# Performance work log

Measured on AMD Instinct MI355X. Metric: run time of the kernel, lower is better.

Reference implementation:

```python
import jax, jax.numpy as jnp
import numpy as np

DILATIONS = (3, 6, 12, 18, 24)
B, C, H, W = 16, 26, 96, 72
INNER = 128
EPS = 1e-5


def conv2d(x, w, padding=0, dilation=1):
    return jax.lax.conv_general_dilated(
        x, w, window_strides=(1, 1),
        padding=[(padding, padding), (padding, padding)],
        rhs_dilation=(dilation, dilation),
        dimension_numbers=('NCHW', 'OIHW', 'NCHW'))


def batch_norm(x, p):
    # p: [4, C] rows = (scale, bias, running_mean, running_var); eval-mode BN
    s, b, m, v = p[0], p[1], p[2], p[3]
    inv = s * jax.lax.rsqrt(v + EPS)
    return x * inv[None, :, None, None] + (b - m * inv)[None, :, None, None]


def basic_block(x, w1, p1, w2, p2, wd=None, pd=None):
    h = jax.nn.relu(batch_norm(conv2d(x, w1, padding=1), p1))
    h = batch_norm(conv2d(h, w2, padding=1), p2)
    idn = x if wd is None else batch_norm(conv2d(x, wd), pd)
    return jax.nn.relu(h + idn)


def _bilinear(img, py, px):
    # img: [cpg, H, W]; py, px: [K, H, W] sample coords; zero outside bounds
    Hi, Wi = img.shape[1], img.shape[2]
    y0f = jnp.floor(py); x0f = jnp.floor(px)
    ly = py - y0f; lx = px - x0f
    y0 = y0f.astype(jnp.int32); x0 = x0f.astype(jnp.int32)

    def gather(yi, xi):
        valid = ((yi >= 0) & (yi < Hi) & (xi >= 0) & (xi < Wi)).astype(img.dtype)
        return img[:, jnp.clip(yi, 0, Hi - 1), jnp.clip(xi, 0, Wi - 1)] * valid[None]

    return (gather(y0, x0) * ((1 - ly) * (1 - lx))[None]
            + gather(y0, x0 + 1) * ((1 - ly) * lx)[None]
            + gather(y0 + 1, x0) * (ly * (1 - lx))[None]
            + gather(y0 + 1, x0 + 1) * (ly * lx)[None])


def deform_conv(x, offset, w, dil):
    # x: [B,C,H,W]; offset: [B, dg*2*K, H, W] ((dy,dx) interleaved per kernel tap);
    # w: [O,C,3,3]; stride 1, padding = dil -> same spatial size
    Bn, Cn, Hn, Wn = x.shape
    K = w.shape[2] * w.shape[3]
    dg = offset.shape[1] // (2 * K)
    cpg = Cn // dg
    off = offset.reshape(Bn, dg, K, 2, Hn, Wn)
    ky = jnp.arange(K) // 3 - 1
    kx = jnp.arange(K) % 3 - 1
    base_y = (jnp.arange(Hn)[None, :] + ky[:, None] * dil).astype(x.dtype)  # [K,H]
    base_x = (jnp.arange(Wn)[None, :] + kx[:, None] * dil).astype(x.dtype)  # [K,W]
    py = base_y[None, None, :, :, None] + off[:, :, :, 0]  # [B,dg,K,H,W]
    px = base_x[None, None, :, None, :] + off[:, :, :, 1]
    xg = x.reshape(Bn, dg, cpg, Hn, Wn)
    samp = jax.vmap(jax.vmap(_bilinear))(xg, py, px)  # [B,dg,cpg,K,H,W]
    vals = samp.reshape(Bn, Cn, K, Hn, Wn)
    return jnp.einsum('bckij,ock->boij', vals, w.reshape(w.shape[0], Cn, K))


def setup_inputs():
    key = jax.random.key(0)
    ks = jax.random.split(key, 14)
    std = 0.001  # matches nn.init.normal_(std=0.001)

    def bnp(k, c):
        k1, k2, k3, k4 = jax.random.split(k, 4)
        return jnp.stack([jax.random.uniform(k1, (c,), minval=0.5, maxval=1.5),
                          jax.random.normal(k2, (c,)) * 0.1,
                          jax.random.normal(k3, (c,)) * 0.1,
                          jax.random.uniform(k4, (c,), minval=0.5, maxval=1.5)])

    return {
        'ref_x': jax.random.normal(ks[0], (B, C, H, W), jnp.float32),
        'sup_x': jax.random.normal(ks[1], (B, C, H, W), jnp.float32),
        'w1_0': jax.random.normal(ks[2], (INNER, C, 3, 3), jnp.float32) * std,
        'w2_0': jax.random.normal(ks[3], (INNER, INNER, 3, 3), jnp.float32) * std,
        'wd_0': jax.random.normal(ks[4], (INNER, C, 1, 1), jnp.float32) * std,
        'bn1_0': bnp(ks[5], INNER),
        'bn2_0': bnp(ks[6], INNER),
        'bnd_0': bnp(ks[7], INNER),
        'w1_rest': jax.random.normal(ks[8], (19, INNER, INNER, 3, 3), jnp.float32) * std,
        'w2_rest': jax.random.normal(ks[9], (19, INNER, INNER, 3, 3), jnp.float32) * std,
        'bn1_rest': jnp.stack([bnp(k, INNER) for k in jax.random.split(ks[10], 19)]),
        'bn2_rest': jnp.stack([bnp(k, INNER) for k in jax.random.split(ks[11], 19)]),
        'offset_ws': jax.random.normal(ks[12], (5, C * 2 * 9, INNER, 3, 3), jnp.float32) * std,
        'deform_ws': jax.random.normal(ks[13], (5, C, C, 3, 3), jnp.float32) * std,
    }


def reference(ref_x, sup_x, w1_0, w2_0, wd_0, bn1_0, bn2_0, bnd_0,
              w1_rest, w2_rest, bn1_rest, bn2_rest, offset_ws, deform_ws):
    # offset feature chain: 20 BasicBlocks on (ref - sup)
    h = basic_block(ref_x - sup_x, w1_0, bn1_0, w2_0, bn2_0, wd_0, bnd_0)
    for t in range(19):
        h = basic_block(h, w1_rest[t], bn1_rest[t], w2_rest[t], bn2_rest[t])
    # 5 dilation branches: dilated offset conv -> deformable conv on sup_x; average
    out = jnp.zeros_like(sup_x)
    for i, dil in enumerate(DILATIONS):
        off = conv2d(h, offset_ws[i], padding=dil, dilation=dil)
        out = out + deform_conv(sup_x, off, deform_ws[i], dil)
    return out / len(DILATIONS)
```

## Files before the change

kernel.cpp:

```cpp
#include <hip/hip_runtime.h>

typedef unsigned short u16;
typedef unsigned int u32;
typedef __bf16 bf16x8 __attribute__((ext_vector_type(8)));
typedef float f32x4 __attribute__((ext_vector_type(4)));

#define NB 16
#define CIN 26
#define IMH 96
#define IMW 72
#define HW6912 6912
#define NPIX 110592
#define SPH 98
#define SPW 74
#define SPAD 1

__device__ __forceinline__ float b2f(u16 h) {
    union { u32 u; float f; } x; x.u = ((u32)h) << 16; return x.f;
}
__device__ __forceinline__ u16 f2b(float f) {
    union { float f; u32 u; } x; x.f = f;
    u32 u = x.u;
    u32 r = (u + 0x7fffu + ((u >> 16) & 1u)) >> 16;
    return (u16)r;
}
__device__ __forceinline__ float ldin(const void* p, int i, int f) {
    return f ? ((const float*)p)[i] : b2f(((const u16*)p)[i]);
}

__device__ __forceinline__ int pbase(int m, int clog2) {
    int b = m / HW6912;
    int p = m - b * HW6912;
    int y = p / IMW;
    int x = p - y * IMW;
    return (((b * SPH + y + SPAD) * SPW) + (x + SPAD)) << clog2;
}

__device__ __forceinline__ void glds16(const u16* g, u16* l) {
    __builtin_amdgcn_global_load_lds(
        (const __attribute__((address_space(1))) void*)g,
        (__attribute__((address_space(3))) void*)l, 16, 0, 0);
}

__global__ void probe_kernel(const void* bn, int* flag) {
    if (threadIdx.x == 0 && blockIdx.x == 0) {
        const float* f = (const float*)bn;
        int cnt = 0;
        for (int j = 64; j < 128; ++j) {
            float v = f[j];
            if (v >= 0.4f && v <= 1.6f) cnt++;
        }
        *flag = (cnt >= 32) ? 1 : 0;
    }
}

__global__ __launch_bounds__(256) void zero_ws_kernel(uint4* p, int n16) {
    int i = blockIdx.x * 256 + threadIdx.x;
    int stride = gridDim.x * 256;
    for (; i < n16; i += stride) p[i] = make_uint4(0u, 0u, 0u, 0u);
}

__global__ __launch_bounds__(256) void fill_x0_kernel(const void* __restrict__ ref,
                                                      const void* __restrict__ sup,
                                                      u16* __restrict__ x0,
                                                      const int* __restrict__ flag) {
    int f = *flag;
    int t = blockIdx.x * 256 + threadIdx.x;
    int b = t / HW6912;
    int p = t - b * HW6912;
    int y = p / IMW;
    int x = p - y * IMW;
    int dst = ((b * SPH + y + SPAD) * SPW + (x + SPAD)) << 5;
    #pragma unroll 1
    for (int c = 0; c < CIN; ++c) {
        int src = (b * CIN + c) * HW6912 + p;
        x0[dst + c] = f2b(ldin(ref, src, f) - ldin(sup, src, f));
    }
}

__global__ __launch_bounds__(256) void prep_rest_kernel(const void* __restrict__ w1r,
                                                        const void* __restrict__ w2r,
                                                        const void* __restrict__ bn1r,
                                                        const void* __restrict__ bn2r,
                                                        u16* __restrict__ dst,
                                                        const int* __restrict__ flag) {
    int f = *flag;
    int idx = blockIdx.x * 256 + threadIdx.x;
    int c = idx / 147456;
    int e = idx - c * 147456;
    int ee = e & 7;
    int l = (e >> 3) & 63;
    int j = (e >> 9) & 1;
    int w2 = (e >> 10) & 1;
    int rest = e >> 11;
    int it = rest % 36;
    int nt = rest / 36;
    int n = nt * 64 + w2 * 32 + j * 16 + (l & 15);
    int k = it * 32 + ((l >> 4) << 3) + ee;
    int s = k >> 7, ci = k & 127;
    const void* w  = (c < 19) ? w1r : w2r;
    int wb         = ((c < 19) ? c : (c - 19)) * 147456;
    const void* bn = (c < 19) ? bn1r : bn2r;
    int bb         = ((c < 19) ? c : (c - 19)) * 512;
    float inv = ldin(bn, bb + n, f) * rsqrtf(ldin(bn, bb + 384 + n, f) + 1e-5f);
    dst[idx] = f2b(ldin(w, wb + (n * 128 + ci) * 9 + s, f) * inv);
}

__global__ __launch_bounds__(256) void prep_b0_kernel(const void* __restrict__ w1_0,
                                                      const void* __restrict__ w2_0,
                                                      const void* __restrict__ wd_0,
                                                      const void* __restrict__ bn1_0,
                                                      const void* __restrict__ bn2_0,
                                                      const void* __restrict__ bnd_0,
                                                      u16* __restrict__ W20,
                                                      u16* __restrict__ W10,
                                                      u16* __restrict__ Wd,
                                                      const int* __restrict__ flag) {
    int f = *flag;
    int idx = blockIdx.x * 256 + threadIdx.x;
    if (idx < 147456) {
        int e = idx;
        int ee = e & 7;
        int l = (e >> 3) & 63;
        int j = (e >> 9) & 1;
        int w2 = (e >> 10) & 1;
        int rest = e >> 11;
        int it = rest % 36;
        int nt = rest / 36;
        int n = nt * 64 + w2 * 32 + j * 16 + (l & 15);
        int k = it * 32 + ((l >> 4) << 3) + ee;
        int s = k >> 7, ci = k & 127;
        float inv = ldin(bn2_0, n, f) * rsqrtf(ldin(bn2_0, 384 + n, f) + 1e-5f);
        W20[idx] = f2b(ldin(w2_0, (n * 128 + ci) * 9 + s, f) * inv);
    } else if (idx < 184320) {
        int j = idx - 147456;
        int o = j / 288, k = j - o * 288;
        int s = k >> 5, ci = k & 31;
        float inv = ldin(bn1_0, o, f) * rsqrtf(ldin(bn1_0, 384 + o, f) + 1e-5f);
        W10[j] = (ci < CIN) ? f2b(ldin(w1_0, (o * CIN + ci) * 9 + s, f) * inv) : (u16)0;
    } else {
        int j = idx - 184320;
        int o = j >> 5, ci = j & 31;
        float inv = ldin(bnd_0, o, f) * rsqrtf(ldin(bnd_0, 384 + o, f) + 1e-5f);
        Wd[j] = (ci < CIN) ? f2b(ldin(wd_0, o * CIN + ci, f) * inv) : (u16)0;
    }
}

__global__ __launch_bounds__(256) void prep_off_kernel(const void* __restrict__ offw,
                                                       u16* __restrict__ dst,
                                                       const int* __restrict__ flag) {
    int f = *flag;
    int idx = blockIdx.x * 256 + threadIdx.x;
    int e = idx & 7;
    int l = (idx >> 3) & 63;
    int j = (idx >> 9) & 1;
    int w2 = (idx >> 10) & 1;
    int rest = idx >> 11;
    int it = rest % 36;
    int dnt = rest / 36;
    int nt = dnt & 7;
    int d = dnt >> 3;
    int n = nt * 64 + w2 * 32 + j * 16 + (l & 15);
    int k = it * 32 + (l >> 4) * 8 + e;
    int s = k >> 7, ci = k & 127;
    dst[idx] = (n < 468) ? f2b(ldin(offw, ((d * 468 + n) * 128 + ci) * 9 + s, f)) : (u16)0;
}

__global__ __launch_bounds__(256) void prep_dw_kernel(const void* __restrict__ dwall,
                                                      float* __restrict__ dst,
                                                      const int* __restrict__ flag) {
    int f = *flag;
    int idx = blockIdx.x * 256 + threadIdx.x;
    if (idx >= 32760) return;
    int d = idx / 6552;
    int r = idx - d * 6552;
    int o = r % 28;
    int ct = r / 28;
    int c = ct / 9, t = ct - c * 9;
    dst[idx] = (o < CIN) ? ldin(dwall, d * 6084 + (o * CIN + c) * 9 + t, f) : 0.f;
}

__global__ __launch_bounds__(256) void prep_bias_kernel(const void* __restrict__ bn1_0,
                                                        const void* __restrict__ bn2_0,
                                                        const void* __restrict__ bnd_0,
                                                        const void* __restrict__ bn1r,
                                                        const void* __restrict__ bn2r,
                                                        float* __restrict__ dst,
                                                        const int* __restrict__ flag) {
    int f = *flag;
    int idx = blockIdx.x * 256 + threadIdx.x;
    if (idx >= 41 * 128) return;
    int set = idx >> 7;
    int o = idx & 127;
    const void* bn; int bb = 0;
    if (set == 0) bn = bn1_0;
    else if (set == 1) bn = bn2_0;
    else if (set == 2) bn = bnd_0;
    else if (set < 22) { bn = bn1r; bb = (set - 3) * 512; }
    else { bn = bn2r; bb = (set - 22) * 512; }
    float s = ldin(bn, bb + o, f), b = ldin(bn, bb + 128 + o, f);
    float mu = ldin(bn, bb + 256 + o, f), v = ldin(bn, bb + 384 + o, f);
    float inv = s * rsqrtf(v + 1e-5f);
    dst[idx] = b - mu * inv;
}

__global__ __launch_bounds__(256) void conv_gemm(const u16* __restrict__ A,
                                                 const u16* __restrict__ W,
                                                 const float* __restrict__ bias,
                                                 u16* __restrict__ out,
                                                 int clog2, int nslab, int K,
                                                 int relu) {
    __shared__ u16 As[2][128 * 32];
    __shared__ u16 Bs[2][64 * 32];
    int tid = threadIdx.x;
    int m0 = blockIdx.x * 128;
    int n0 = blockIdx.y * 64;
    int Cin = 1 << clog2;

    int r0 = tid >> 2;
    int q8 = (tid & 3) * 8;
    int arow0 = pbase(m0 + r0, clog2) + q8;
    int arow1 = pbase(m0 + r0 + 64, clog2) + q8;
    int brow0 = (n0 + r0) * K + q8;
    int l8 = tid * 8;

    f32x4 acc[4][2];
    #pragma unroll
    for (int i = 0; i < 4; ++i)
        #pragma unroll
        for (int j = 0; j < 2; ++j)
            acc[i][j] = (f32x4){0.f, 0.f, 0.f, 0.f};

    int wid = tid >> 6;
    int wm = (wid >> 1) * 64;
    int wn = (wid & 1) * 32;
    int lane = tid & 63;
    int lr = lane & 15;
    int lq = lane >> 4;

    int nk = K >> 5;
    auto stage = [&](int buf, int kt) {
        int sl = kt >> clog2;
        int win = kt & (Cin - 1);
        int soff = 0;
        if (nslab == 9) {
            int d3 = sl / 3;
            soff = (((d3 - 1) * SPW + (sl - d3 * 3 - 1))) << clog2;
        }
        glds16(A + arow0 + soff + win, &As[buf][l8]);
        glds16(A + arow1 + soff + win, &As[buf][2048 + l8]);
        glds16(W + brow0 + kt, &Bs[buf][l8]);
    };

    stage(0, 0);
    #pragma unroll 1
    for (int it = 0; it < nk; ++it) {
        __syncthreads();
        if (it + 1 < nk) stage((it + 1) & 1, (it + 1) << 5);
        const u16* as = As[it & 1];
        const u16* bs = Bs[it & 1];
        bf16x8 af[4], bfr[2];
        #pragma unroll
        for (int i = 0; i < 4; ++i)
            af[i] = *(const bf16x8*)&as[(wm + i * 16 + lr) * 32 + lq * 8];
        #pragma unroll
        for (int j = 0; j < 2; ++j)
            bfr[j] = *(const bf16x8*)&bs[(wn + j * 16 + lr) * 32 + lq * 8];
        #pragma unroll
        for (int i = 0; i < 4; ++i)
            #pragma unroll
            for (int j = 0; j < 2; ++j)
                acc[i][j] = __builtin_amdgcn_mfma_f32_16x16x32_bf16(af[i], bfr[j], acc[i][j], 0, 0, 0);
    }

    #pragma unroll
    for (int i = 0; i < 4; ++i) {
        #pragma unroll
        for (int r = 0; r < 4; ++r) {
            int ml = m0 + wm + i * 16 + lq * 4 + r;
            int ob = pbase(ml, 7);
            #pragma unroll
            for (int j = 0; j < 2; ++j) {
                int n = n0 + wn + j * 16 + lr;
                float v = acc[i][j][r] + bias[n];
                if (relu) v = fmaxf(v, 0.f);
                out[ob + n] = f2b(v);
            }
        }
    }
}

__global__ __launch_bounds__(256, 8) void chain_conv(const u16* __restrict__ A,
                                                     const u16* __restrict__ W,
                                                     const float* __restrict__ bias,
                                                     const u16* __restrict__ idn,
                                                     u16* __restrict__ out,
                                                     int relu) {
    __shared__ u16 As[2][128 * 32];
    int tid = threadIdx.x;
    int wg = blockIdx.x;
    int sw = (wg & 7) * 216 + (wg >> 3);
    int mt = sw >> 1, nt = sw & 1;
    int m0 = mt * 128, n0 = nt * 64;

    int r0 = tid >> 2;
    int q8 = (tid & 3) * 8;
    int pbq[2];
    #pragma unroll
    for (int q = 0; q < 2; ++q) {
        int p = m0 + r0 + q * 64;
        int b = p / HW6912;
        int rem = p - b * HW6912;
        int y = rem / IMW;
        int x = rem - y * IMW;
        pbq[q] = ((b * SPH + y + 1) * SPW + (x + 1)) * 128;
    }
    int l8 = tid * 8;

    f32x4 acc[4][2];
    #pragma unroll
    for (int i = 0; i < 4; ++i) {
        acc[i][0] = (f32x4){0.f, 0.f, 0.f, 0.f};
        acc[i][1] = (f32x4){0.f, 0.f, 0.f, 0.f};
    }

    int wid = tid >> 6;
    int wm = (wid >> 1) * 64;
    int w2 = wid & 1;
    int wn = w2 * 32;
    int lane = tid & 63;
    int lr = lane & 15;
    int lq = lane >> 4;

    const u16* wv = W + nt * 73728 + w2 * 1024 + lane * 8;

    auto stage = [&](int buf, int kt) {
        int sl = kt >> 7;
        int win = kt & 127;
        int d3 = sl / 3;
        int soff = ((d3 - 1) * SPW + (sl - d3 * 3 - 1)) * 128;
        glds16(A + pbq[0] + soff + win + q8, &As[buf][l8]);
        glds16(A + pbq[1] + soff + win + q8, &As[buf][2048 + l8]);
    };

    stage(0, 0);
    #pragma unroll 1
    for (int it = 0; it < 36; ++it) {
        __syncthreads();
        if (it + 1 < 36) stage((it + 1) & 1, (it + 1) << 5);
        const u16* as = As[it & 1];
        bf16x8 af[4], bfr[2];
        #pragma unroll
        for (int i = 0; i < 4; ++i)
            af[i] = *(const bf16x8*)&as[(wm + i * 16 + lr) * 32 + lq * 8];
        bfr[0] = *(const bf16x8*)(wv + it * 2048);
        bfr[1] = *(const bf16x8*)(wv + it * 2048 + 512);
        #pragma unroll
        for (int i = 0; i < 4; ++i)
            #pragma unroll
            for (int j = 0; j < 2; ++j)
                acc[i][j] = __builtin_amdgcn_mfma_f32_16x16x32_bf16(af[i], bfr[j], acc[i][j], 0, 0, 0);
    }

    #pragma unroll
    for (int i = 0; i < 4; ++i) {
        #pragma unroll
        for (int r = 0; r < 4; ++r) {
            int ml = m0 + wm + i * 16 + lq * 4 + r;
            int ob = pbase(ml, 7);
            #pragma unroll
            for (int j = 0; j < 2; ++j) {
                int n = n0 + wn + j * 16 + lr;
                float v = acc[i][j][r] + bias[n];
                if (idn) v += b2f(idn[ob + n]);
                if (relu) v = fmaxf(v, 0.f);
                out[ob + n] = f2b(v);
            }
        }
    }
}

__global__ __launch_bounds__(256, 8) void off_conv(const u16* __restrict__ A,
                                                   const u16* __restrict__ W,
                                                   u16* __restrict__ out,
                                                   int dil, int m_base) {
    __shared__ u16 As[2][128 * 32];
    int tid = threadIdx.x;
    int wg = blockIdx.x;
    int sw = (wg & 7) * 216 + (wg >> 3);
    int mt = sw >> 3, nt = sw & 7;
    int m0 = mt * 128, n0 = nt * 64;

    int r0 = tid >> 2;
    int q8 = (tid & 3) * 8;
    int pb2[2], py[2], px[2];
    #pragma unroll
    for (int q = 0; q < 2; ++q) {
        int p = m_base + m0 + r0 + q * 64;
        int b = p / HW6912;
        int rem = p - b * HW6912;
        pb2[q] = b;
        py[q] = rem / IMW;
        px[q] = rem - py[q] * IMW;
    }
    int l8 = tid * 8;

    f32x4 acc[4][2];
    #pragma unroll
    for (int i = 0; i < 4; ++i) {
        acc[i][0] = (f32x4){0.f, 0.f, 0.f, 0.f};
        acc[i][1] = (f32x4){0.f, 0.f, 0.f, 0.f};
    }

    int wid = tid >> 6;
    int wm = (wid >> 1) * 64;
    int wn = (wid & 1) * 32;
    int lane = tid & 63;
    int lr = lane & 15;
    int lq = lane >> 4;

    const u16* wv = W + nt * 73728 + (wid & 1) * 1024 + lane * 8;

    auto stage = [&](int buf, int kt) {
        int sl = kt >> 7;
        int win = kt & 127;
        int d3 = sl / 3;
        int dy = (d3 - 1) * dil, dx = (sl - d3 * 3 - 1) * dil;
        #pragma unroll
        for (int q = 0; q < 2; ++q) {
            int y2 = py[q] + dy, x2 = px[q] + dx;
            uint4 v = make_uint4(0u, 0u, 0u, 0u);
            if (y2 >= 0 && y2 < IMH && x2 >= 0 && x2 < IMW)
                v = *(const uint4*)(A + ((pb2[q] * SPH + y2 + 1) * SPW + x2 + 1) * 128 + win + q8);
            *(uint4*)&As[buf][q * 2048 + l8] = v;
        }
    };

    stage(0, 0);
    #pragma unroll 1
    for (int it = 0; it < 36; ++it) {
        __syncthreads();
        if (it + 1 < 36) stage((it + 1) & 1, (it + 1) << 5);
        const u16* as = As[it & 1];
        bf16x8 af[4], bfr[2];
        #pragma unroll
        for (int i = 0; i < 4; ++i)
            af[i] = *(const bf16x8*)&as[(wm + i * 16 + lr) * 32 + lq * 8];
        bfr[0] = *(const bf16x8*)(wv + it * 2048);
        bfr[1] = *(const bf16x8*)(wv + it * 2048 + 512);
        #pragma unroll
        for (int i = 0; i < 4; ++i)
            #pragma unroll
            for (int j = 0; j < 2; ++j)
                acc[i][j] = __builtin_amdgcn_mfma_f32_16x16x32_bf16(af[i], bfr[j], acc[i][j], 0, 0, 0);
    }

    #pragma unroll
    for (int i = 0; i < 4; ++i) {
        #pragma unroll
        for (int r = 0; r < 4; ++r) {
            int ml = m0 + wm + i * 16 + lq * 4 + r;
            int ob = ml * 468;
            #pragma unroll
            for (int j = 0; j < 2; ++j) {
                int n = n0 + wn + j * 16 + lr;
                if (n < 468) out[ob + n] = f2b(acc[i][j][r]);
            }
        }
    }
}

template <int F>
__device__ __forceinline__ float dsamp2(const void* sup, int base, int yi, int xi) {
    bool ok = (yi >= 0) & (yi < IMH) & (xi >= 0) & (xi < IMW);
    int yc = yi < 0 ? 0 : (yi > IMH - 1 ? IMH - 1 : yi);
    int xc = xi < 0 ? 0 : (xi > IMW - 1 ? IMW - 1 : xi);
    float v = F ? ((const float*)sup)[base + yc * IMW + xc]
                : b2f(((const u16*)sup)[base + yc * IMW + xc]);
    return ok ? v : 0.f;
}

template <int F>
__device__ __forceinline__ void deform_body(const void* __restrict__ sup,
                                            const u16* __restrict__ oc,
                                            const float* __restrict__ wsm,
                                            f32x4 acc[7],
                                            int c0, int c1, int b, int y, int x, int dil) {
    #pragma unroll 1
    for (int c = c0; c < c1; ++c) {
        int ibase = (b * CIN + c) * HW6912;
        #pragma unroll
        for (int t = 0; t < 9; ++t) {
            u32 pr = *(const u32*)(oc + c * 18 + t * 2);
            float dy = b2f((u16)(pr & 0xffffu));
            float dx = b2f((u16)(pr >> 16));
            float py = (float)(y + (t / 3 - 1) * dil) + dy;
            float px = (float)(x + (t % 3 - 1) * dil) + dx;
            float y0f = floorf(py), x0f = floorf(px);
            float ly = py - y0f, lx = px - x0f;
            int y0 = (int)y0f, x0 = (int)x0f;
            float v00 = dsamp2<F>(sup, ibase, y0, x0);
            float v01 = dsamp2<F>(sup, ibase, y0, x0 + 1);
            float v10 = dsamp2<F>(sup, ibase, y0 + 1, x0);
            float v11 = dsamp2<F>(sup, ibase, y0 + 1, x0 + 1);
            float val = (v00 * (1.f - lx) + v01 * lx) * (1.f - ly)
                      + (v10 * (1.f - lx) + v11 * lx) * ly;
            const float4* wr = (const float4*)&wsm[(c * 9 + t) * 28];
            #pragma unroll
            for (int u = 0; u < 7; ++u) {
                float4 w4 = wr[u];
                acc[u][0] = fmaf(val, w4.x, acc[u][0]);
                acc[u][1] = fmaf(val, w4.y, acc[u][1]);
                acc[u][2] = fmaf(val, w4.z, acc[u][2]);
                acc[u][3] = fmaf(val, w4.w, acc[u][3]);
            }
        }
    }
}

__global__ __launch_bounds__(256) void deform_kernel(const void* __restrict__ sup,
                                                     const u16* __restrict__ offb,
                                                     const float* __restrict__ wsp,
                                                     float* __restrict__ accws,
                                                     int dil, int first, int m_base,
                                                     const int* __restrict__ flag) {
    int f = *flag;
    __shared__ alignas(16) float wsm[26 * 9 * 28];
    __shared__ float red[4 * 32 * 27];
    int tid = threadIdx.x;
    int bid = blockIdx.x;
    int sw = (bid & 7) * 108 + (bid >> 3);
    for (int i = tid; i < 1638; i += 256)
        ((float4*)wsm)[i] = ((const float4*)wsp)[i];
    __syncthreads();

    int px = tid & 31;
    int cg = tid >> 5;
    int c0 = (cg * 26) >> 3;
    int c1 = ((cg + 1) * 26) >> 3;
    int ml = sw * 32 + px;
    int m = m_base + ml;
    int b = m / HW6912;
    int p = m - b * HW6912;
    int y = p / IMW;
    int x = p - y * IMW;

    f32x4 acc[7];
    #pragma unroll
    for (int u = 0; u < 7; ++u) acc[u] = (f32x4){0.f, 0.f, 0.f, 0.f};

    const u16* oc = offb + (size_t)ml * 468;
    if (f) deform_body<1>(sup, oc, wsm, acc, c0, c1, b, y, x, dil);
    else   deform_body<0>(sup, oc, wsm, acc, c0, c1, b, y, x, dil);

    #pragma unroll
    for (int u = 0; u < 7; ++u)
        #pragma unroll
        for (int k2 = 0; k2 < 4; ++k2) {
            float v = acc[u][k2];
            acc[u][k2] = v + __shfl_xor(v, 32);
        }

    int w = tid >> 6;
    if (!(tid & 32)) {
        float* mr = red + (w * 32 + px) * 27;
        #pragma unroll
        for (int u = 0; u < 7; ++u)
            #pragma unroll
            for (int k2 = 0; k2 < 4; ++k2) {
                int o = u * 4 + k2;
                if (o < 26) mr[o] = acc[u][k2];
            }
    }
    __syncthreads();

    int base_m = m_base + sw * 32;
    for (int v = tid; v < 32 * 26; v += 256) {
        int ppx = v / 26;
        int o = v - ppx * 26;
        float s = red[(0 * 32 + ppx) * 27 + o] + red[(1 * 32 + ppx) * 27 + o]
                + red[(2 * 32 + ppx) * 27 + o] + red[(3 * 32 + ppx) * 27 + o];
        size_t ai = (size_t)(base_m + ppx) * 32 + o;
        if (first) accws[ai] = s;
        else       accws[ai] += s;
    }
}

__global__ __launch_bounds__(256) void finalize_kernel(const float* __restrict__ accws,
                                                       void* __restrict__ out,
                                                       const int* __restrict__ flag) {
    int f = *flag;
    int q = blockIdx.x * 256 + threadIdx.x;
    int b = q / (CIN * HW6912);
    int r = q - b * (CIN * HW6912);
    int o = r / HW6912;
    int p = r - o * HW6912;
    float v = accws[(size_t)(b * HW6912 + p) * 32 + o] * 0.2f;
    if (f) ((float*)out)[q] = v;
    else   ((u16*)out)[q] = f2b(v);
}

extern "C" void kernel_launch(void* const* d_in, const int* in_sizes, int n_in,
                              void* d_out, int out_size, void* d_ws, size_t ws_size,
                              hipStream_t stream) {
    (void)in_sizes; (void)n_in; (void)out_size;
    const void* ref_x    = d_in[0];
    const void* sup_x    = d_in[1];
    const void* w1_0     = d_in[2];
    const void* w2_0     = d_in[3];
    const void* wd_0     = d_in[4];
    const void* bn1_0    = d_in[5];
    const void* bn2_0    = d_in[6];
    const void* bnd_0    = d_in[7];
    const void* w1_rest  = d_in[8];
    const void* w2_rest  = d_in[9];
    const void* bn1_rest = d_in[10];
    const void* bn2_rest = d_in[11];
    const void* offset_w = d_in[12];
    const void* deform_w = d_in[13];

    size_t o_x0    = 0;
    size_t o_h0    = o_x0 + 7426048;
    size_t o_h1s   = o_h0 + 29704192;
    size_t o_acc   = o_h1s + 29704192;
    size_t o_wrest = o_acc + 14155776;
    size_t o_w20   = o_wrest + 11206656;
    size_t o_w10   = o_w20 + 294912;
    size_t o_wd    = o_w10 + 73728;
    size_t o_woff  = o_wd + 8192;
    size_t o_bias  = o_woff + 5898240;
    size_t o_wsall = o_bias + 20992;
    size_t o_flag  = o_wsall + 131072;
    size_t o_end   = o_flag + 64;
    if (ws_size < o_end) return;

    char* ws = (char*)d_ws;
    u16* x0    = (u16*)(ws + o_x0);
    u16* h0    = (u16*)(ws + o_h0);
    u16* offb  = (u16*)(ws + o_h0);
    u16* h1s   = (u16*)(ws + o_h1s);
    float* accb = (float*)(ws + o_acc);
    u16* Wr    = (u16*)(ws + o_wrest);
    u16* W20   = (u16*)(ws + o_w20);
    u16* W10   = (u16*)(ws + o_w10);
    u16* Wd    = (u16*)(ws + o_wd);
    u16* Woff  = (u16*)(ws + o_woff);
    float* biasb = (float*)(ws + o_bias);
    float* wsall = (float*)(ws + o_wsall);
    int* flagp = (int*)(ws + o_flag);

    dim3 blk(256);

    probe_kernel<<<1, 64, 0, stream>>>(bn1_0, flagp);
    zero_ws_kernel<<<2048, blk, 0, stream>>>((uint4*)ws, (int)((7426048 + 2 * 29704192) / 16));
    fill_x0_kernel<<<432, blk, 0, stream>>>(ref_x, sup_x, x0, flagp);
    prep_rest_kernel<<<21888, blk, 0, stream>>>(w1_rest, w2_rest, bn1_rest, bn2_rest, Wr, flagp);
    prep_b0_kernel<<<736, blk, 0, stream>>>(w1_0, w2_0, wd_0, bn1_0, bn2_0, bnd_0, W20, W10, Wd, flagp);
    prep_off_kernel<<<11520, blk, 0, stream>>>(offset_w, Woff, flagp);
    prep_dw_kernel<<<128, blk, 0, stream>>>(deform_w, wsall, flagp);
    prep_bias_kernel<<<21, blk, 0, stream>>>(bn1_0, bn2_0, bnd_0, bn1_rest, bn2_rest, biasb, flagp);

    conv_gemm<<<dim3(864, 2), blk, 0, stream>>>(x0, Wd, biasb + 2 * 128, h1s, 5, 1, 32, 0);
    conv_gemm<<<dim3(864, 2), blk, 0, stream>>>(x0, W10, biasb + 0 * 128, h0, 5, 9, 288, 1);
    chain_conv<<<1728, blk, 0, stream>>>(h0, W20, biasb + 1 * 128, h1s, h1s, 1);

    for (int t = 0; t < 19; ++t) {
        const u16* wa = Wr + (size_t)t * 147456;
        const u16* wb = Wr + (size_t)(19 + t) * 147456;
        chain_conv<<<1728, blk, 0, stream>>>(h1s, wa, biasb + (3 + t) * 128, nullptr, h0, 1);
        chain_conv<<<1728, blk, 0, stream>>>(h0, wb, biasb + (22 + t) * 128, h1s, h1s, 1);
    }

    const int dils[5] = {3, 6, 12, 18, 24};
    for (int i = 0; i < 5; ++i) {
        for (int cb = 0; cb < 4; ++cb) {
            int mb = cb * 27648;
            off_conv<<<1728, blk, 0, stream>>>(h1s, Woff + (size_t)i * 589824, offb, dils[i], mb);
            deform_kernel<<<864, blk, 0, stream>>>(sup_x, offb, wsall + (size_t)i * 6552,
                                                   accb, dils[i], (i == 0) ? 1 : 0, mb, flagp);
        }
    }
    finalize_kernel<<<11232, blk, 0, stream>>>(accb, d_out, flagp);
}
```

Baseline: 3.952 ms.

## Widen chain_conv tile to full 128 output channels and swizzle LDS A tile

```diff
diff --git a/kernel.cpp b/kernel.cpp
--- a/kernel.cpp
+++ b/kernel.cpp
@@ -290,7 +290,7 @@
     }
 }
 
-__global__ __launch_bounds__(256, 8) void chain_conv(const u16* __restrict__ A,
+__global__ __launch_bounds__(256, 4) void chain_conv(const u16* __restrict__ A,
                                                      const u16* __restrict__ W,
                                                      const float* __restrict__ bias,
                                                      const u16* __restrict__ idn,
@@ -299,12 +299,11 @@
     __shared__ u16 As[2][128 * 32];
     int tid = threadIdx.x;
     int wg = blockIdx.x;
-    int sw = (wg & 7) * 216 + (wg >> 3);
-    int mt = sw >> 1, nt = sw & 1;
-    int m0 = mt * 128, n0 = nt * 64;
+    int mt = (wg & 7) * 108 + (wg >> 3);
+    int m0 = mt * 128;
 
     int r0 = tid >> 2;
-    int q8 = (tid & 3) * 8;
+    int c8 = ((tid & 3) ^ (r0 & 3)) * 8;
     int pbq[2];
     #pragma unroll
     for (int q = 0; q < 2; ++q) {
@@ -317,30 +316,30 @@
     }
     int l8 = tid * 8;
 
-    f32x4 acc[4][2];
-    #pragma unroll
-    for (int i = 0; i < 4; ++i) {
-        acc[i][0] = (f32x4){0.f, 0.f, 0.f, 0.f};
-        acc[i][1] = (f32x4){0.f, 0.f, 0.f, 0.f};
-    }
+    f32x4 acc[4][4];
+    #pragma unroll
+    for (int i = 0; i < 4; ++i)
+        #pragma unroll
+        for (int jj = 0; jj < 4; ++jj)
+            acc[i][jj] = (f32x4){0.f, 0.f, 0.f, 0.f};
 
     int wid = tid >> 6;
     int wm = (wid >> 1) * 64;
-    int w2 = wid & 1;
-    int wn = w2 * 32;
+    int wn2 = wid & 1;
     int lane = tid & 63;
     int lr = lane & 15;
     int lq = lane >> 4;
-
-    const u16* wv = W + nt * 73728 + w2 * 1024 + lane * 8;
+    int rchunk = (lq ^ (lr & 3)) * 8;
+
+    const u16* wv = W + wn2 * 73728 + lane * 8;
 
     auto stage = [&](int buf, int kt) {
         int sl = kt >> 7;
         int win = kt & 127;
         int d3 = sl / 3;
         int soff = ((d3 - 1) * SPW + (sl - d3 * 3 - 1)) * 128;
-        glds16(A + pbq[0] + soff + win + q8, &As[buf][l8]);
-        glds16(A + pbq[1] + soff + win + q8, &As[buf][2048 + l8]);
+        glds16(A + pbq[0] + soff + win + c8, &As[buf][l8]);
+        glds16(A + pbq[1] + soff + win + c8, &As[buf][2048 + l8]);
     };
 
     stage(0, 0);
@@ -349,17 +348,18 @@
         __syncthreads();
         if (it + 1 < 36) stage((it + 1) & 1, (it + 1) << 5);
         const u16* as = As[it & 1];
-        bf16x8 af[4], bfr[2];
+        bf16x8 af[4], bfr[4];
         #pragma unroll
         for (int i = 0; i < 4; ++i)
-            af[i] = *(const bf16x8*)&as[(wm + i * 16 + lr) * 32 + lq * 8];
-        bfr[0] = *(const bf16x8*)(wv + it * 2048);
-        bfr[1] = *(const bf16x8*)(wv + it * 2048 + 512);
+            af[i] = *(const bf16x8*)&as[(wm + i * 16 + lr) * 32 + rchunk];
+        #pragma unroll
+        for (int jj = 0; jj < 4; ++jj)
+            bfr[jj] = *(const bf16x8*)(wv + it * 2048 + jj * 512);
         #pragma unroll
         for (int i = 0; i < 4; ++i)
             #pragma unroll
-            for (int j = 0; j < 2; ++j)
-                acc[i][j] = __builtin_amdgcn_mfma_f32_16x16x32_bf16(af[i], bfr[j], acc[i][j], 0, 0, 0);
+            for (int jj = 0; jj < 4; ++jj)
+                acc[i][jj] = __builtin_amdgcn_mfma_f32_16x16x32_bf16(af[i], bfr[jj], acc[i][jj], 0, 0, 0);
     }
 
     #pragma unroll
@@ -369,9 +369,9 @@
             int ml = m0 + wm + i * 16 + lq * 4 + r;
             int ob = pbase(ml, 7);
             #pragma unroll
-            for (int j = 0; j < 2; ++j) {
-                int n = n0 + wn + j * 16 + lr;
-                float v = acc[i][j][r] + bias[n];
+            for (int jj = 0; jj < 4; ++jj) {
+                int n = wn2 * 64 + jj * 16 + lr;
+                float v = acc[i][jj][r] + bias[n];
                 if (idn) v += b2f(idn[ob + n]);
                 if (relu) v = fmaxf(v, 0.f);
                 out[ob + n] = f2b(v);
@@ -662,13 +662,13 @@
 
     conv_gemm<<<dim3(864, 2), blk, 0, stream>>>(x0, Wd, biasb + 2 * 128, h1s, 5, 1, 32, 0);
     conv_gemm<<<dim3(864, 2), blk, 0, stream>>>(x0, W10, biasb + 0 * 128, h0, 5, 9, 288, 1);
-    chain_conv<<<1728, blk, 0, stream>>>(h0, W20, biasb + 1 * 128, h1s, h1s, 1);
+    chain_conv<<<864, blk, 0, stream>>>(h0, W20, biasb + 1 * 128, h1s, h1s, 1);
 
     for (int t = 0; t < 19; ++t) {
         const u16* wa = Wr + (size_t)t * 147456;
         const u16* wb = Wr + (size_t)(19 + t) * 147456;
-        chain_conv<<<1728, blk, 0, stream>>>(h1s, wa, biasb + (3 + t) * 128, nullptr, h0, 1);
-        chain_conv<<<1728, blk, 0, stream>>>(h0, wb, biasb + (22 + t) * 128, h1s, h1s, 1);
+        chain_conv<<<864, blk, 0, stream>>>(h1s, wa, biasb + (3 + t) * 128, nullptr, h0, 1);
+        chain_conv<<<864, blk, 0, stream>>>(h0, wb, biasb + (22 + t) * 128, h1s, h1s, 1);
     }
 
     const int dils[5] = {3, 6, 12, 18, 24};
```

Result: faster. 3.723 ms (-5.8%).
